# Kernel optimization log

Hardware: AMD Instinct MI355X
Metric: run time of the kernel (lower is better)

Reference implementation:

```python
import jax, jax.numpy as jnp
import numpy as np

N = 50000
E = 600000
F_IN = 128
HID = 128
N_CLS = 16


def setup_inputs() -> dict:
    key = jax.random.key(0)
    ks = jax.random.split(key, 12)
    x = jax.random.normal(ks[0], (N, F_IN), dtype=jnp.float32)
    edge_index = jax.random.randint(ks[1], (2, E), 0, N, dtype=jnp.int64)
    def glorot(k, shape):
        lim = float(np.sqrt(6.0 / (shape[0] + shape[1])))
        return jax.random.uniform(k, shape, jnp.float32, -lim, lim)
    return {
        "x": x,
        "edge_index": edge_index,
        "W1": glorot(ks[2], (F_IN, HID)), "b1": jnp.zeros((HID,), jnp.float32),
        "W2": glorot(ks[3], (HID, HID)), "b2": jnp.zeros((HID,), jnp.float32),
        "W3": glorot(ks[4], (HID, HID)), "b3": jnp.zeros((HID,), jnp.float32),
        "Wlin": glorot(ks[5], (HID, N_CLS)), "blin": jnp.zeros((N_CLS,), jnp.float32),
    }


def _gcn_norm(edge_index, n_nodes):
    # PyG GCNConv default: add self-loops, symmetric normalization
    loops = jnp.arange(n_nodes, dtype=edge_index.dtype)
    src = jnp.concatenate([edge_index[0], loops])  # [E+N]
    dst = jnp.concatenate([edge_index[1], loops])  # [E+N]
    deg = jax.ops.segment_sum(jnp.ones_like(dst, dtype=jnp.float32), dst,
                              num_segments=n_nodes)
    dis = jnp.where(deg > 0, jax.lax.rsqrt(jnp.maximum(deg, 1.0)), 0.0)
    norm = dis[src] * dis[dst]  # [E+N]
    return src, dst, norm


def _gcn_conv(h, src, dst, norm, n_nodes, W, b):
    h = h @ W                                   # transform first (small GEMM)
    msg = h[src] * norm[:, None]                # gather + scale, [E+N, HID]
    out = jax.ops.segment_sum(msg, dst, num_segments=n_nodes)  # scatter-add
    return out + b


def reference(x, edge_index, W1, b1, W2, b2, W3, b3, Wlin, blin):
    n_nodes = x.shape[0]
    src, dst, norm = _gcn_norm(edge_index, n_nodes)
    h = jax.nn.relu(_gcn_conv(x, src, dst, norm, n_nodes, W1, b1))
    h = jax.nn.relu(_gcn_conv(h, src, dst, norm, n_nodes, W2, b2))
    h = _gcn_conv(h, src, dst, norm, n_nodes, W3, b3)
    return h @ Wlin + blin  # [N, N_CLS]
```

## Files before the change

### kernel.cpp

```cpp
#include <hip/hip_runtime.h>
#include <hip/hip_fp16.h>


#define FD 128
#define NCLS 16

__global__ __launch_bounds__(256) void k_init_deg(int* __restrict__ degi, int n) {
  int i = blockIdx.x * 256 + threadIdx.x;
  if (i < n) degi[i] = 1;
}

__global__ __launch_bounds__(256) void k_count(const int* __restrict__ dst,
                                               int* __restrict__ degi, int e) {
  int i = blockIdx.x * 256 + threadIdx.x;
  if (i < e) atomicAdd(&degi[dst[i]], 1);
}

__global__ __launch_bounds__(256) void k_dis(const int* __restrict__ degi,
                                             float* __restrict__ dis, int n) {
  int i = blockIdx.x * 256 + threadIdx.x;
  if (i < n) dis[i] = rsqrtf((float)degi[i]);
}

__global__ __launch_bounds__(1024) void k_scanA(const int* __restrict__ degi,
                                                int* __restrict__ ptr,
                                                int* __restrict__ bsum, int n) {
  __shared__ int buf[1024];
  int tid = threadIdx.x;
  int i = blockIdx.x * 1024 + tid;
  int v = (i < n) ? (degi[i] - 1) : 0;
  buf[tid] = v;
  __syncthreads();
  for (int off = 1; off < 1024; off <<= 1) {
    int t = (tid >= off) ? buf[tid - off] : 0;
    __syncthreads();
    buf[tid] += t;
    __syncthreads();
  }
  if (i < n) ptr[i] = buf[tid] - v;
  if (tid == 1023) bsum[blockIdx.x] = buf[1023];
}

__global__ void k_scanB(int* __restrict__ bsum, int nb) {
  if (threadIdx.x == 0 && blockIdx.x == 0) {
    int run = 0;
    for (int b = 0; b < nb; ++b) { int t = bsum[b]; bsum[b] = run; run += t; }
  }
}

__global__ __launch_bounds__(256) void k_scanC(int* __restrict__ ptr,
                                               int* __restrict__ cur,
                                               const int* __restrict__ bsum,
                                               int n, int e) {
  int i = blockIdx.x * 256 + threadIdx.x;
  if (i < n) {
    int p = ptr[i] + bsum[i >> 10];
    ptr[i] = p;
    cur[i] = p;
  }
  if (i == 0) ptr[n] = e;
}

__global__ __launch_bounds__(256) void k_fill(const int* __restrict__ src,
                                              const int* __restrict__ dst,
                                              int* __restrict__ cur,
                                              const float* __restrict__ dis,
                                              int2* __restrict__ sn, int e) {
  int i = blockIdx.x * 256 + threadIdx.x;
  if (i < e) {
    int s = src[i], d = dst[i];
    int p = atomicAdd(&cur[d], 1);
    sn[p] = make_int2(s, __float_as_int(dis[s] * dis[d]));
  }
}

__global__ __launch_bounds__(256) void k_gemm128h(const float* __restrict__ in,
                                                  const float* __restrict__ W,
                                                  __half* __restrict__ outh, int n) {
  __shared__ float4 wl[FD][16];
  int tid = threadIdx.x;
  int cbase = blockIdx.y * 64;
  int cb4 = cbase >> 2;
  const float4* W4 = reinterpret_cast<const float4*>(W);
  for (int i = tid; i < FD * 16; i += 256) {
    int k = i >> 4, cg = i & 15;
    wl[k][cg] = W4[k * 32 + cb4 + cg];
  }
  __syncthreads();

  int cg = tid & 15;
  int rg = tid >> 4;
  int rbase = blockIdx.x * 64 + rg * 4;
  const float* rowp[4];
#pragma unroll
  for (int r = 0; r < 4; ++r) {
    int row = rbase + r;
    if (row > n - 1) row = n - 1;
    rowp[r] = in + (size_t)row * FD;
  }
  float4 acc[4];
#pragma unroll
  for (int r = 0; r < 4; ++r) acc[r] = make_float4(0.f, 0.f, 0.f, 0.f);

  float4 a_cur[4];
#pragma unroll
  for (int r = 0; r < 4; ++r) a_cur[r] = *reinterpret_cast<const float4*>(rowp[r]);

  for (int k = 0; k < FD; k += 4) {
    int kn = (k + 4 < FD) ? k + 4 : k;
    float4 a_nxt[4];
#pragma unroll
    for (int r = 0; r < 4; ++r)
      a_nxt[r] = *reinterpret_cast<const float4*>(rowp[r] + kn);
    float4 w0 = wl[k + 0][cg];
    float4 w1 = wl[k + 1][cg];
    float4 w2 = wl[k + 2][cg];
    float4 w3 = wl[k + 3][cg];
#pragma unroll
    for (int r = 0; r < 4; ++r) {
      float4 a = a_cur[r];
      acc[r].x = fmaf(a.x, w0.x, acc[r].x);
      acc[r].y = fmaf(a.x, w0.y, acc[r].y);
      acc[r].z = fmaf(a.x, w0.z, acc[r].z);
      acc[r].w = fmaf(a.x, w0.w, acc[r].w);
      acc[r].x = fmaf(a.y, w1.x, acc[r].x);
      acc[r].y = fmaf(a.y, w1.y, acc[r].y);
      acc[r].z = fmaf(a.y, w1.z, acc[r].z);
      acc[r].w = fmaf(a.y, w1.w, acc[r].w);
      acc[r].x = fmaf(a.z, w2.x, acc[r].x);
      acc[r].y = fmaf(a.z, w2.y, acc[r].y);
      acc[r].z = fmaf(a.z, w2.z, acc[r].z);
      acc[r].w = fmaf(a.z, w2.w, acc[r].w);
      acc[r].x = fmaf(a.w, w3.x, acc[r].x);
      acc[r].y = fmaf(a.w, w3.y, acc[r].y);
      acc[r].z = fmaf(a.w, w3.z, acc[r].z);
      acc[r].w = fmaf(a.w, w3.w, acc[r].w);
      a_cur[r] = a_nxt[r];
    }
  }

#pragma unroll
  for (int r = 0; r < 4; ++r) {
    int row = rbase + r;
    if (row < n) {
      __half h[4];
      h[0] = __float2half_rn(acc[r].x);
      h[1] = __float2half_rn(acc[r].y);
      h[2] = __float2half_rn(acc[r].z);
      h[3] = __float2half_rn(acc[r].w);
      *reinterpret_cast<uint2*>(&outh[(size_t)row * FD + cbase + cg * 4]) =
          *reinterpret_cast<uint2*>(h);
    }
  }
}

__device__ __forceinline__ float agg_acc(const __half* __restrict__ t,
                                         const int* __restrict__ ptr,
                                         const int2* __restrict__ sn,
                                         const float* __restrict__ dis,
                                         int node, int f) {
  float d = dis[node];
  float acc = __half2float(t[(size_t)node * FD + f]) * (d * d);
  int e0 = ptr[node], e1 = ptr[node + 1];
  for (int e = e0; e < e1; e += 16) {
    int s[16];
    float w[16];
#pragma unroll
    for (int j = 0; j < 16; ++j) {
      if (e + j < e1) {
        int2 p = sn[e + j];
        s[j] = p.x;
        w[j] = __int_as_float(p.y);
      } else {
        s[j] = node;
        w[j] = 0.f;
      }
    }
    __half v[16];
#pragma unroll
    for (int j = 0; j < 16; ++j) v[j] = t[(size_t)s[j] * FD + f];
#pragma unroll
    for (int j = 0; j < 16; ++j) acc = fmaf(__half2float(v[j]), w[j], acc);
  }
  return acc;
}

__global__ __launch_bounds__(128) void k_agg(const __half* __restrict__ t,
                                             const int* __restrict__ ptr,
                                             const int2* __restrict__ sn,
                                             const float* __restrict__ dis,
                                             const float* __restrict__ bias,
                                             float* __restrict__ out, int relu) {
  int node = blockIdx.x;
  int f = threadIdx.x;
  float acc = agg_acc(t, ptr, sn, dis, node, f) + bias[f];
  if (relu) acc = fmaxf(acc, 0.f);
  out[(size_t)node * FD + f] = acc;
}

__global__ __launch_bounds__(128) void k_agg_lin(const __half* __restrict__ t,
                                                 const int* __restrict__ ptr,
                                                 const int2* __restrict__ sn,
                                                 const float* __restrict__ dis,
                                                 const float* __restrict__ b3,
                                                 const float* __restrict__ Wl,
                                                 const float* __restrict__ bl,
                                                 float* __restrict__ out) {
  __shared__ float hl[FD];
  __shared__ float part[8][NCLS];
  int node = blockIdx.x;
  int f = threadIdx.x;
  hl[f] = agg_acc(t, ptr, sn, dis, node, f) + b3[f];
  __syncthreads();
  int c = f & 15, p = f >> 4;
  float s = 0.f;
#pragma unroll
  for (int k = 0; k < 16; ++k)
    s = fmaf(hl[p * 16 + k], Wl[(p * 16 + k) * NCLS + c], s);
  part[p][c] = s;
  __syncthreads();
  if (f < NCLS) {
    float r = bl[f];
#pragma unroll
    for (int q = 0; q < 8; ++q) r += part[q][f];
    out[node * NCLS + f] = r;
  }
}

extern "C" void kernel_launch(void* const* d_in, const int* in_sizes, int n_in,
                              void* d_out, int out_size, void* d_ws, size_t ws_size,
                              hipStream_t stream) {
  const float* x  = (const float*)d_in[0];
  const int*   ei = (const int*)d_in[1];
  const float* W1 = (const float*)d_in[2];
  const float* b1 = (const float*)d_in[3];
  const float* W2 = (const float*)d_in[4];
  const float* b2 = (const float*)d_in[5];
  const float* W3 = (const float*)d_in[6];
  const float* b3 = (const float*)d_in[7];
  const float* Wl = (const float*)d_in[8];
  const float* bl = (const float*)d_in[9];
  float* out = (float*)d_out;

  const int n = in_sizes[0] / FD;
  const int e = in_sizes[1] / 2;
  const int* src = ei;
  const int* dst = ei + e;

  __half* th  = (__half*)d_ws;
  float* bufH = (float*)(th + (size_t)n * FD);
  int*   degi = (int*)(bufH + (size_t)n * FD);
  float* dis  = (float*)(degi + n);
  int*   ptr  = (int*)(dis + n);
  int*   cur  = ptr + n + 1;
  int*   bsum = cur + n;
  int2*  sn   = (int2*)(((uintptr_t)(bsum + 64) + 15) & ~(uintptr_t)15);

  const int gn = (n + 255) / 256;
  const int ge = (e + 255) / 256;
  const int nb = (n + 1023) / 1024;

  k_init_deg<<<gn, 256, 0, stream>>>(degi, n);
  k_count<<<ge, 256, 0, stream>>>(dst, degi, e);
  k_dis<<<gn, 256, 0, stream>>>(degi, dis, n);
  k_scanA<<<nb, 1024, 0, stream>>>(degi, ptr, bsum, n);
  k_scanB<<<1, 64, 0, stream>>>(bsum, nb);
  k_scanC<<<gn, 256, 0, stream>>>(ptr, cur, bsum, n, e);
  k_fill<<<ge, 256, 0, stream>>>(src, dst, cur, dis, sn, e);

  dim3 gG((n + 63) / 64, 2);

  k_gemm128h<<<gG, 256, 0, stream>>>(x, W1, th, n);
  k_agg<<<n, 128, 0, stream>>>(th, ptr, sn, dis, b1, bufH, 1);
  k_gemm128h<<<gG, 256, 0, stream>>>(bufH, W2, th, n);
  k_agg<<<n, 128, 0, stream>>>(th, ptr, sn, dis, b2, bufH, 1);
  k_gemm128h<<<gG, 256, 0, stream>>>(bufH, W3, th, n);
  k_agg_lin<<<n, 128, 0, stream>>>(th, ptr, sn, dis, b3, Wl, bl, out);
}
```

Baseline: 386.5 us.

## Aggregate one node per wavefront with vectorized half4 gathers and split edges

Restructures the CSR aggregation so each 64-lane wavefront handles one node. The two half-waves process alternate edges, and each lane gathers 4 fp16 features through ushort4 loads. The partial sums are then combined with a cross-half shuffle. Blocks now hold 4 nodes with 256 threads instead of one node per 128-thread block, and the final linear layer reduces with shuffles instead of a second shared-memory stage. The goal is fewer, wider memory transactions and less per-block overhead. The grid size n/4 assumes n is divisible by 4, and there is no bounds check on node.

```diff
diff --git a/kernel.cpp b/kernel.cpp
--- a/kernel.cpp
+++ b/kernel.cpp
@@ -154,21 +154,22 @@
   }
 }
 
-__device__ __forceinline__ float agg_acc(const __half* __restrict__ t,
+__device__ __forceinline__ void agg_wave(const __half* __restrict__ t,
                                          const int* __restrict__ ptr,
                                          const int2* __restrict__ sn,
-                                         const float* __restrict__ dis,
-                                         int node, int f) {
-  float d = dis[node];
-  float acc = __half2float(t[(size_t)node * FD + f]) * (d * d);
+                                         int node, int lane, float o[4]) {
+  int h = lane >> 5;
+  int q = lane & 31;
+  float a0 = 0.f, a1 = 0.f, a2 = 0.f, a3 = 0.f;
   int e0 = ptr[node], e1 = ptr[node + 1];
-  for (int e = e0; e < e1; e += 16) {
-    int s[16];
-    float w[16];
-#pragma unroll
-    for (int j = 0; j < 16; ++j) {
-      if (e + j < e1) {
-        int2 p = sn[e + j];
+  for (int base = e0; base < e1; base += 16) {
+    int s[8];
+    float w[8];
+#pragma unroll
+    for (int j = 0; j < 8; ++j) {
+      int idx = base + 2 * j + h;
+      if (idx < e1) {
+        int2 p = sn[idx];
         s[j] = p.x;
         w[j] = __int_as_float(p.y);
       } else {
@@ -176,29 +177,56 @@
         w[j] = 0.f;
       }
     }
-    __half v[16];
-#pragma unroll
-    for (int j = 0; j < 16; ++j) v[j] = t[(size_t)s[j] * FD + f];
-#pragma unroll
-    for (int j = 0; j < 16; ++j) acc = fmaf(__half2float(v[j]), w[j], acc);
-  }
-  return acc;
-}
-
-__global__ __launch_bounds__(128) void k_agg(const __half* __restrict__ t,
+    ushort4 v[8];
+#pragma unroll
+    for (int j = 0; j < 8; ++j)
+      v[j] = *reinterpret_cast<const ushort4*>(&t[(size_t)s[j] * FD + q * 4]);
+#pragma unroll
+    for (int j = 0; j < 8; ++j) {
+      a0 = fmaf(__half2float(__ushort_as_half(v[j].x)), w[j], a0);
+      a1 = fmaf(__half2float(__ushort_as_half(v[j].y)), w[j], a1);
+      a2 = fmaf(__half2float(__ushort_as_half(v[j].z)), w[j], a2);
+      a3 = fmaf(__half2float(__ushort_as_half(v[j].w)), w[j], a3);
+    }
+  }
+  o[0] = a0 + __shfl(a0, lane ^ 32, 64);
+  o[1] = a1 + __shfl(a1, lane ^ 32, 64);
+  o[2] = a2 + __shfl(a2, lane ^ 32, 64);
+  o[3] = a3 + __shfl(a3, lane ^ 32, 64);
+}
+
+__global__ __launch_bounds__(256) void k_agg(const __half* __restrict__ t,
                                              const int* __restrict__ ptr,
                                              const int2* __restrict__ sn,
                                              const float* __restrict__ dis,
                                              const float* __restrict__ bias,
                                              float* __restrict__ out, int relu) {
-  int node = blockIdx.x;
-  int f = threadIdx.x;
-  float acc = agg_acc(t, ptr, sn, dis, node, f) + bias[f];
-  if (relu) acc = fmaxf(acc, 0.f);
-  out[(size_t)node * FD + f] = acc;
-}
-
-__global__ __launch_bounds__(128) void k_agg_lin(const __half* __restrict__ t,
+  int lane = threadIdx.x & 63;
+  int node = blockIdx.x * 4 + (threadIdx.x >> 6);
+  float d = dis[node];
+  float dd = d * d;
+  float o[4];
+  agg_wave(t, ptr, sn, node, lane, o);
+  if (lane < 32) {
+    int q = lane;
+    ushort4 sv = *reinterpret_cast<const ushort4*>(&t[(size_t)node * FD + q * 4]);
+    float4 b = *reinterpret_cast<const float4*>(&bias[q * 4]);
+    o[0] = fmaf(__half2float(__ushort_as_half(sv.x)), dd, o[0]) + b.x;
+    o[1] = fmaf(__half2float(__ushort_as_half(sv.y)), dd, o[1]) + b.y;
+    o[2] = fmaf(__half2float(__ushort_as_half(sv.z)), dd, o[2]) + b.z;
+    o[3] = fmaf(__half2float(__ushort_as_half(sv.w)), dd, o[3]) + b.w;
+    if (relu) {
+      o[0] = fmaxf(o[0], 0.f);
+      o[1] = fmaxf(o[1], 0.f);
+      o[2] = fmaxf(o[2], 0.f);
+      o[3] = fmaxf(o[3], 0.f);
+    }
+    float4 r = make_float4(o[0], o[1], o[2], o[3]);
+    *reinterpret_cast<float4*>(&out[(size_t)node * FD + q * 4]) = r;
+  }
+}
+
+__global__ __launch_bounds__(256) void k_agg_lin(const __half* __restrict__ t,
                                                  const int* __restrict__ ptr,
                                                  const int2* __restrict__ sn,
                                                  const float* __restrict__ dis,
@@ -206,25 +234,35 @@
                                                  const float* __restrict__ Wl,
                                                  const float* __restrict__ bl,
                                                  float* __restrict__ out) {
-  __shared__ float hl[FD];
-  __shared__ float part[8][NCLS];
-  int node = blockIdx.x;
-  int f = threadIdx.x;
-  hl[f] = agg_acc(t, ptr, sn, dis, node, f) + b3[f];
+  __shared__ float hl[4][FD];
+  int wid = threadIdx.x >> 6;
+  int lane = threadIdx.x & 63;
+  int node = blockIdx.x * 4 + wid;
+  float d = dis[node];
+  float dd = d * d;
+  float o[4];
+  agg_wave(t, ptr, sn, node, lane, o);
+  if (lane < 32) {
+    int q = lane;
+    ushort4 sv = *reinterpret_cast<const ushort4*>(&t[(size_t)node * FD + q * 4]);
+    float4 b = *reinterpret_cast<const float4*>(&b3[q * 4]);
+    hl[wid][q * 4 + 0] = fmaf(__half2float(__ushort_as_half(sv.x)), dd, o[0]) + b.x;
+    hl[wid][q * 4 + 1] = fmaf(__half2float(__ushort_as_half(sv.y)), dd, o[1]) + b.y;
+    hl[wid][q * 4 + 2] = fmaf(__half2float(__ushort_as_half(sv.z)), dd, o[2]) + b.z;
+    hl[wid][q * 4 + 3] = fmaf(__half2float(__ushort_as_half(sv.w)), dd, o[3]) + b.w;
+  }
   __syncthreads();
-  int c = f & 15, p = f >> 4;
+  int c = lane & 15, kc = lane >> 4;
   float s = 0.f;
 #pragma unroll
-  for (int k = 0; k < 16; ++k)
-    s = fmaf(hl[p * 16 + k], Wl[(p * 16 + k) * NCLS + c], s);
-  part[p][c] = s;
-  __syncthreads();
-  if (f < NCLS) {
-    float r = bl[f];
-#pragma unroll
-    for (int q = 0; q < 8; ++q) r += part[q][f];
-    out[node * NCLS + f] = r;
-  }
+  for (int k0 = 0; k0 < 32; ++k0) {
+    int k = kc * 32 + k0;
+    s = fmaf(hl[wid][k], Wl[k * NCLS + c], s);
+  }
+  s += __shfl(s, lane ^ 16, 64);
+  s += __shfl(s, lane ^ 32, 64);
+  if (lane < NCLS)
+    out[(size_t)node * NCLS + lane] = s + bl[lane];
 }
 
 extern "C" void kernel_launch(void* const* d_in, const int* in_sizes, int n_in,
@@ -269,11 +307,12 @@
   k_fill<<<ge, 256, 0, stream>>>(src, dst, cur, dis, sn, e);
 
   dim3 gG((n + 63) / 64, 2);
+  const int ga = n / 4;
 
   k_gemm128h<<<gG, 256, 0, stream>>>(x, W1, th, n);
-  k_agg<<<n, 128, 0, stream>>>(th, ptr, sn, dis, b1, bufH, 1);
+  k_agg<<<ga, 256, 0, stream>>>(th, ptr, sn, dis, b1, bufH, 1);
   k_gemm128h<<<gG, 256, 0, stream>>>(bufH, W2, th, n);
-  k_agg<<<n, 128, 0, stream>>>(th, ptr, sn, dis, b2, bufH, 1);
+  k_agg<<<ga, 256, 0, stream>>>(th, ptr, sn, dis, b2, bufH, 1);
   k_gemm128h<<<gG, 256, 0, stream>>>(bufH, W3, th, n);
-  k_agg_lin<<<n, 128, 0, stream>>>(th, ptr, sn, dis, b3, Wl, bl, out);
-}
+  k_agg_lin<<<ga, 256, 0, stream>>>(th, ptr, sn, dis, b3, Wl, bl, out);
+}
```

Result: faster. 374.2 us (-3.2%).
